# Optimization experiments

Measured on AMD Instinct MI355X. Metric: run time of the kernel, lower is better.

## Reference

```python
import jax, jax.numpy as jnp
import numpy as np
from math import sqrt

B, LQ, LK = 4, 256, 50000
EDGE_IN, NODE_IN, OUT = 128, 128, 256
KV_IN = NODE_IN + EDGE_IN  # 256


def setup_inputs() -> dict:
    key = jax.random.key(0)
    ks = jax.random.split(key, 8)
    s = 0.05
    return {
        "query": jax.random.normal(ks[0], (B, LQ, EDGE_IN), jnp.float32),
        "input": jax.random.normal(ks[1], (B, LK, KV_IN), jnp.float32),
        "Wq": jax.random.normal(ks[2], (OUT, EDGE_IN), jnp.float32) * s,
        "bq": jax.random.normal(ks[3], (OUT,), jnp.float32) * s,
        "Wk": jax.random.normal(ks[4], (OUT, KV_IN), jnp.float32) * s,
        "bk": jax.random.normal(ks[5], (OUT,), jnp.float32) * s,
        "Wv": jax.random.normal(ks[6], (OUT, KV_IN), jnp.float32) * s,
        "bv": jax.random.normal(ks[7], (OUT,), jnp.float32) * s,
    }


def reference(query, input, Wq, bq, Wk, bk, Wv, bv):
    norm = 1.0 / sqrt(OUT)
    Q = query @ Wq.T + bq            # [B, LQ, OUT]
    K = input @ Wk.T + bk            # [B, LK, OUT]
    V = input @ Wv.T + bv            # [B, LK, OUT]
    alpha = jnp.einsum("bqd,bkd->bqk", Q, K) * norm  # [B, LQ, LK]
    alpha = jax.nn.softmax(alpha, axis=-1)
    # z = alpha^T * V broadcasts only because LQ == OUT:
    # out[b, j] = sum_k alpha[b, j, k] * V[b, k, j]
    return jnp.einsum("bqk,bkq->bq", alpha, V)      # [B, OUT]
```

## Files before the change

### kernel.cpp

```cpp
#include <hip/hip_runtime.h>
#include <hip/hip_bf16.h>
#include <stdint.h>

using f32x4  = __attribute__((ext_vector_type(4))) float;
using bf16x8 = __attribute__((ext_vector_type(8))) short;

constexpr int BATCH = 4;
constexpr int LQ_   = 256;
constexpr int LK_   = 50000;
constexpr int OUTD  = 256;
constexpr int EIN   = 128;
constexpr int TR    = 16;
constexpr int NT    = LK_ / TR;
constexpr int KCH   = 64;

__device__ __forceinline__ uint32_t f2bf(float f) {
  uint32_t u = __builtin_bit_cast(uint32_t, f);
  u = (u + 0x7fffu + ((u >> 16) & 1u)) >> 16;
  return u;
}

__device__ __forceinline__ void block_sync_lds() {
  asm volatile("s_waitcnt lgkmcnt(0)" ::: "memory");
  __builtin_amdgcn_sched_barrier(0);
  __builtin_amdgcn_s_barrier();
  __builtin_amdgcn_sched_barrier(0);
}

__global__ __launch_bounds__(256) void prep_all(
    const float* __restrict__ query, const float* __restrict__ Wq,
    const float* __restrict__ bq,    const float* __restrict__ Wk,
    const float* __restrict__ Wv,    ushort* __restrict__ Gn,
    ushort* __restrict__ Wvbf,       float* __restrict__ numden)
{
  const int blk = blockIdx.x, tid = threadIdx.x;
  if (blk >= 64) {
    if (blk < 96) {
      int base = (blk - 64) * 2048 + tid * 8;
      float4 a = *(const float4*)(Wv + base);
      float4 c = *(const float4*)(Wv + base + 4);
      uint4 pk;
      pk.x = f2bf(a.x) | (f2bf(a.y) << 16);
      pk.y = f2bf(a.z) | (f2bf(a.w) << 16);
      pk.z = f2bf(c.x) | (f2bf(c.y) << 16);
      pk.w = f2bf(c.z) | (f2bf(c.w) << 16);
      *(uint4*)(Wvbf + base) = pk;
    } else {
      for (int i = tid; i < 2 * BATCH * OUTD; i += 256) numden[i] = 0.f;
    }
    return;
  }
  __shared__ float qin[16 * EIN];
  __shared__ float Qr [16 * OUTD];
  const int b = blk >> 4, q0 = (blk & 15) * 16;
  {
    int idx = tid * 8;
    int row = idx >> 7, c = idx & 127;
    const float* p = query + ((size_t)b * LQ_ + q0 + row) * EIN + c;
    float4 a = *(const float4*)p;
    float4 d = *(const float4*)(p + 4);
    float* q = &qin[row * EIN + c];
    q[0]=a.x; q[1]=a.y; q[2]=a.z; q[3]=a.w; q[4]=d.x; q[5]=d.y; q[6]=d.z; q[7]=d.w;
  }
  __syncthreads();

  float acc[16];
  {
    float bias = bq[tid];
#pragma unroll
    for (int i = 0; i < 16; ++i) acc[i] = bias;
  }
  for (int d4 = 0; d4 < EIN / 4; ++d4) {
    f32x4 w4 = *(const f32x4*)(Wq + tid * EIN + d4 * 4);
#pragma unroll
    for (int i = 0; i < 16; ++i) {
      f32x4 q4 = *(const f32x4*)(qin + i * EIN + d4 * 4);
      acc[i] += q4[0]*w4[0] + q4[1]*w4[1] + q4[2]*w4[2] + q4[3]*w4[3];
    }
  }
#pragma unroll
  for (int i = 0; i < 16; ++i) Qr[i * OUTD + tid] = acc[i];
  __syncthreads();

  float acc2[16];
#pragma unroll
  for (int i = 0; i < 16; ++i) acc2[i] = 0.f;
  for (int d4 = 0; d4 < OUTD / 4; ++d4) {
    float w0 = Wk[(d4*4+0) * OUTD + tid];
    float w1 = Wk[(d4*4+1) * OUTD + tid];
    float w2 = Wk[(d4*4+2) * OUTD + tid];
    float w3 = Wk[(d4*4+3) * OUTD + tid];
#pragma unroll
    for (int i = 0; i < 16; ++i) {
      f32x4 q4 = *(const f32x4*)(Qr + i * OUTD + d4 * 4);
      acc2[i] += q4[0]*w0 + q4[1]*w1 + q4[2]*w2 + q4[3]*w3;
    }
  }
  const float norm = 0.0625f;
#pragma unroll
  for (int i = 0; i < 16; ++i)
    Gn[((size_t)b * LQ_ + q0 + i) * OUTD + tid] = (ushort)f2bf(acc2[i] * norm);
}

__global__ __launch_bounds__(1024, 4) void attn_main(
    const float*  __restrict__ input, const ushort* __restrict__ Gn,
    const ushort* __restrict__ Wvbf,  float* __restrict__ num,
    float* __restrict__ den)
{
  __shared__ ushort in_lds[2 * 4096];
  const int idx = blockIdx.x;
  const int b = idx >> 6, kch = idx & (KCH - 1);
  const int t0 = (kch * NT) >> 6, t1 = ((kch + 1) * NT) >> 6;
  const int tid = threadIdx.x, w = tid >> 6, l = tid & 63;
  const int lg = l >> 4, lr = l & 15;
  const float* src = input + (size_t)b * LK_ * 256;

  const int arow = w * 16 + lr;
  const ushort* gp = Gn   + ((size_t)b * LQ_ + arow) * 256 + lg * 8;
  const ushort* vp = Wvbf + (size_t)arow * 256 + lg * 8;
  bf16x8 ga[8], wa[8];
#pragma unroll
  for (int k = 0; k < 8; ++k) {
    ga[k] = *(const bf16x8*)(gp + k * 32);
    wa[k] = *(const bf16x8*)(vp + k * 32);
    asm volatile("" : "+v"(ga[k]), "+v"(wa[k]));
  }

  float numr[4], denr[4];
#pragma unroll
  for (int r = 0; r < 4; ++r) { numr[r] = 0.f; denr[r] = 0.f; }

  const int sg = tid >> 1, sh = tid & 1;
  const int srow = sg >> 5, sfbg = sg & 31;
  float4 s0;
  auto loadreg = [&](int t) {
    const float* p = src + (size_t)(t * TR + srow) * 256 + sfbg * 8 + sh * 4;
    s0 = *(const float4*)p;
  };
  auto writebuf = [&](int buf) {
    char* base = (char*)in_lds + buf * 8192;
    uint2 pk;
    pk.x = f2bf(s0.x) | (f2bf(s0.y) << 16);
    pk.y = f2bf(s0.z) | (f2bf(s0.w) << 16);
    *(uint2*)(base + sfbg * 256 + ((srow ^ (sfbg & 15)) << 4) + sh * 8) = pk;
  };

  loadreg(t0);
  writebuf(t0 & 1);
  loadreg(t0 + 1);
  block_sync_lds();

  for (int t = t0; t < t1; ++t) {
    const char* bbuf = (const char*)in_lds + (t & 1) * 8192;
    f32x4 aS = {0,0,0,0};
    f32x4 aV = {0,0,0,0};
#pragma unroll
    for (int ks = 0; ks < 8; ++ks) {
      const int fb = ks * 4 + lg;
      bf16x8 bb = *(const bf16x8*)(bbuf + fb * 256 + ((lr ^ (fb & 15)) << 4));
      aS = __builtin_amdgcn_mfma_f32_16x16x32_bf16(ga[ks], bb, aS, 0, 0, 0);
      aV = __builtin_amdgcn_mfma_f32_16x16x32_bf16(wa[ks], bb, aV, 0, 0, 0);
    }
#pragma unroll
    for (int r = 0; r < 4; ++r) {
      float e = __expf(aS[r]);
      denr[r] += e;
      numr[r] += e * aV[r];
    }
    if (t + 1 < t1) {
      writebuf((t + 1) & 1);
      if (t + 2 < t1) loadreg(t + 2);
    }
    block_sync_lds();
  }

#pragma unroll
  for (int r = 0; r < 4; ++r) {
    float d_ = denr[r], n_ = numr[r];
#pragma unroll
    for (int m = 1; m < 16; m <<= 1) {
      d_ += __shfl_xor(d_, m, 64);
      n_ += __shfl_xor(n_, m, 64);
    }
    if (lr == 0) {
      int q = w * 16 + lg * 4 + r;
      atomicAdd(&den[b * OUTD + q], d_);
      atomicAdd(&num[b * OUTD + q], n_);
    }
  }
}

__global__ __launch_bounds__(256) void finalize(const float* __restrict__ num,
                                                const float* __restrict__ den,
                                                const float* __restrict__ bv,
                                                float* __restrict__ out) {
  int i = blockIdx.x * 256 + threadIdx.x;
  out[i] = num[i] / den[i] + bv[i & 255];
}

extern "C" void kernel_launch(void* const* d_in, const int* in_sizes, int n_in,
                              void* d_out, int out_size, void* d_ws, size_t ws_size,
                              hipStream_t stream)
{
  const float* query = (const float*)d_in[0];
  const float* input = (const float*)d_in[1];
  const float* Wq    = (const float*)d_in[2];
  const float* bq    = (const float*)d_in[3];
  const float* Wk    = (const float*)d_in[4];
  const float* Wv    = (const float*)d_in[6];
  const float* bv    = (const float*)d_in[7];
  float* out = (float*)d_out;

  char* ws = (char*)d_ws;
  ushort* Gn     = (ushort*)ws;
  ushort* Wvbf   = (ushort*)(ws + 524288);
  float*  numden = (float*)(ws + 524288 + 131072);
  float*  num    = numden;
  float*  den    = numden + BATCH * OUTD;

  prep_all<<<97, 256, 0, stream>>>(query, Wq, bq, Wk, Wv, Gn, Wvbf, numden);
  attn_main<<<BATCH * KCH, 1024, 0, stream>>>(input, Gn, Wvbf, num, den);
  finalize<<<BATCH, 256, 0, stream>>>(num, den, bv, out);
}
```

Before: 105.6 us.

## Split query rows across two 512-thread blocks and use hardware bf16 pack conversion

```diff
diff --git a/kernel.cpp b/kernel.cpp
--- a/kernel.cpp
+++ b/kernel.cpp
@@ -18,6 +18,11 @@
   uint32_t u = __builtin_bit_cast(uint32_t, f);
   u = (u + 0x7fffu + ((u >> 16) & 1u)) >> 16;
   return u;
+}
+__device__ __forceinline__ uint32_t cvtpk(float lo, float hi) {
+  uint32_t r;
+  asm volatile("v_cvt_pk_bf16_f32 %0, %1, %2" : "=v"(r) : "v"(lo), "v"(hi));
+  return r;
 }
 
 __device__ __forceinline__ void block_sync_lds() {
@@ -102,20 +107,20 @@
     Gn[((size_t)b * LQ_ + q0 + i) * OUTD + tid] = (ushort)f2bf(acc2[i] * norm);
 }
 
-__global__ __launch_bounds__(1024, 4) void attn_main(
+__global__ __launch_bounds__(512, 4) void attn_main(
     const float*  __restrict__ input, const ushort* __restrict__ Gn,
     const ushort* __restrict__ Wvbf,  float* __restrict__ num,
     float* __restrict__ den)
 {
   __shared__ ushort in_lds[2 * 4096];
   const int idx = blockIdx.x;
-  const int b = idx >> 6, kch = idx & (KCH - 1);
+  const int b = idx >> 7, qb = (idx >> 6) & 1, kch = idx & (KCH - 1);
   const int t0 = (kch * NT) >> 6, t1 = ((kch + 1) * NT) >> 6;
   const int tid = threadIdx.x, w = tid >> 6, l = tid & 63;
   const int lg = l >> 4, lr = l & 15;
   const float* src = input + (size_t)b * LK_ * 256;
 
-  const int arow = w * 16 + lr;
+  const int arow = qb * 128 + w * 16 + lr;
   const ushort* gp = Gn   + ((size_t)b * LQ_ + arow) * 256 + lg * 8;
   const ushort* vp = Wvbf + (size_t)arow * 256 + lg * 8;
   bf16x8 ga[8], wa[8];
@@ -130,19 +135,24 @@
 #pragma unroll
   for (int r = 0; r < 4; ++r) { numr[r] = 0.f; denr[r] = 0.f; }
 
-  const int sg = tid >> 1, sh = tid & 1;
-  const int srow = sg >> 5, sfbg = sg & 31;
-  float4 s0;
+  const int srow = tid >> 5, sfbg = tid & 31;
+  const float* sbase = src + sfbg * 8;
+  float4 s0, s1;
   auto loadreg = [&](int t) {
-    const float* p = src + (size_t)(t * TR + srow) * 256 + sfbg * 8 + sh * 4;
+    int row = t * TR + srow;
+    row = row < LK_ ? row : LK_ - 1;
+    const float* p = sbase + (size_t)row * 256;
     s0 = *(const float4*)p;
+    s1 = *(const float4*)(p + 4);
   };
   auto writebuf = [&](int buf) {
     char* base = (char*)in_lds + buf * 8192;
-    uint2 pk;
-    pk.x = f2bf(s0.x) | (f2bf(s0.y) << 16);
-    pk.y = f2bf(s0.z) | (f2bf(s0.w) << 16);
-    *(uint2*)(base + sfbg * 256 + ((srow ^ (sfbg & 15)) << 4) + sh * 8) = pk;
+    uint4 pk;
+    pk.x = cvtpk(s0.x, s0.y);
+    pk.y = cvtpk(s0.z, s0.w);
+    pk.z = cvtpk(s1.x, s1.y);
+    pk.w = cvtpk(s1.z, s1.w);
+    *(uint4*)(base + sfbg * 256 + ((srow ^ (sfbg & 15)) << 4)) = pk;
   };
 
   loadreg(t0);
@@ -183,7 +193,7 @@
       n_ += __shfl_xor(n_, m, 64);
     }
     if (lr == 0) {
-      int q = w * 16 + lg * 4 + r;
+      int q = qb * 128 + w * 16 + lg * 4 + r;
       atomicAdd(&den[b * OUTD + q], d_);
       atomicAdd(&num[b * OUTD + q], n_);
     }
@@ -219,6 +229,6 @@
   float*  den    = numden + BATCH * OUTD;
 
   prep_all<<<97, 256, 0, stream>>>(query, Wq, bq, Wk, Wv, Gn, Wvbf, numden);
-  attn_main<<<BATCH * KCH, 1024, 0, stream>>>(input, Gn, Wvbf, num, den);
+  attn_main<<<BATCH * 2 * KCH, 512, 0, stream>>>(input, Gn, Wvbf, num, den);
   finalize<<<BATCH, 256, 0, stream>>>(num, den, bv, out);
 }
```

Result: slower. 109.4 us (+3.6%).

## Fuse finalize into attention via last-block counter; split prep G computation wider

Applied to the files above, without the earlier changes.

```diff
diff --git a/kernel.cpp b/kernel.cpp
--- a/kernel.cpp
+++ b/kernel.cpp
@@ -27,16 +27,17 @@
   __builtin_amdgcn_sched_barrier(0);
 }
 
-__global__ __launch_bounds__(256) void prep_all(
+__global__ __launch_bounds__(256) void prep_fused(
     const float* __restrict__ query, const float* __restrict__ Wq,
     const float* __restrict__ bq,    const float* __restrict__ Wk,
     const float* __restrict__ Wv,    ushort* __restrict__ Gn,
-    ushort* __restrict__ Wvbf,       float* __restrict__ numden)
+    ushort* __restrict__ Wvbf,       float* __restrict__ numden,
+    int* __restrict__ cnt)
 {
   const int blk = blockIdx.x, tid = threadIdx.x;
-  if (blk >= 64) {
-    if (blk < 96) {
-      int base = (blk - 64) * 2048 + tid * 8;
+  if (blk >= 256) {
+    if (blk < 288) {
+      int base = (blk - 256) * 2048 + tid * 8;
       float4 a = *(const float4*)(Wv + base);
       float4 c = *(const float4*)(Wv + base + 4);
       uint4 pk;
@@ -47,12 +48,13 @@
       *(uint4*)(Wvbf + base) = pk;
     } else {
       for (int i = tid; i < 2 * BATCH * OUTD; i += 256) numden[i] = 0.f;
+      if (tid < BATCH) cnt[tid] = 0;
     }
     return;
   }
   __shared__ float qin[16 * EIN];
   __shared__ float Qr [16 * OUTD];
-  const int b = blk >> 4, q0 = (blk & 15) * 16;
+  const int b = blk >> 6, q0 = ((blk >> 2) & 15) * 16, colg = blk & 3;
   {
     int idx = tid * 8;
     int row = idx >> 7, c = idx & 127;
@@ -82,32 +84,27 @@
   for (int i = 0; i < 16; ++i) Qr[i * OUTD + tid] = acc[i];
   __syncthreads();
 
-  float acc2[16];
-#pragma unroll
-  for (int i = 0; i < 16; ++i) acc2[i] = 0.f;
-  for (int d4 = 0; d4 < OUTD / 4; ++d4) {
-    float w0 = Wk[(d4*4+0) * OUTD + tid];
-    float w1 = Wk[(d4*4+1) * OUTD + tid];
-    float w2 = Wk[(d4*4+2) * OUTD + tid];
-    float w3 = Wk[(d4*4+3) * OUTD + tid];
-#pragma unroll
-    for (int i = 0; i < 16; ++i) {
-      f32x4 q4 = *(const f32x4*)(Qr + i * OUTD + d4 * 4);
-      acc2[i] += q4[0]*w0 + q4[1]*w1 + q4[2]*w2 + q4[3]*w3;
-    }
-  }
-  const float norm = 0.0625f;
-#pragma unroll
-  for (int i = 0; i < 16; ++i)
-    Gn[((size_t)b * LQ_ + q0 + i) * OUTD + tid] = (ushort)f2bf(acc2[i] * norm);
+  const int col = colg * 64 + (tid & 63), rg = tid >> 6;
+  float acc2[4] = {0.f, 0.f, 0.f, 0.f};
+  for (int d = 0; d < OUTD; ++d) {
+    float wv = Wk[d * OUTD + col];
+#pragma unroll
+    for (int i = 0; i < 4; ++i) acc2[i] += Qr[(rg * 4 + i) * OUTD + d] * wv;
+  }
+  const float nrm = 1.4426950408889634f * 0.0625f;
+#pragma unroll
+  for (int i = 0; i < 4; ++i)
+    Gn[((size_t)b * LQ_ + q0 + rg * 4 + i) * OUTD + col] = (ushort)f2bf(acc2[i] * nrm);
 }
 
 __global__ __launch_bounds__(1024, 4) void attn_main(
     const float*  __restrict__ input, const ushort* __restrict__ Gn,
     const ushort* __restrict__ Wvbf,  float* __restrict__ num,
-    float* __restrict__ den)
+    float* __restrict__ den,          const float* __restrict__ bv,
+    int* __restrict__ cnt,            float* __restrict__ out)
 {
   __shared__ ushort in_lds[2 * 4096];
+  __shared__ int last_flag;
   const int idx = blockIdx.x;
   const int b = idx >> 6, kch = idx & (KCH - 1);
   const int t0 = (kch * NT) >> 6, t1 = ((kch + 1) * NT) >> 6;
@@ -163,7 +160,7 @@
     }
 #pragma unroll
     for (int r = 0; r < 4; ++r) {
-      float e = __expf(aS[r]);
+      float e = exp2f(aS[r]);
       denr[r] += e;
       numr[r] += e * aV[r];
     }
@@ -188,14 +185,16 @@
       atomicAdd(&num[b * OUTD + q], n_);
     }
   }
-}
-
-__global__ __launch_bounds__(256) void finalize(const float* __restrict__ num,
-                                                const float* __restrict__ den,
-                                                const float* __restrict__ bv,
-                                                float* __restrict__ out) {
-  int i = blockIdx.x * 256 + threadIdx.x;
-  out[i] = num[i] / den[i] + bv[i & 255];
+
+  __threadfence();
+  if (tid == 0)
+    last_flag = (atomicAdd(&cnt[b], 1) == KCH - 1) ? 1 : 0;
+  __syncthreads();
+  if (last_flag && tid < OUTD) {
+    float n_ = atomicAdd(&num[b * OUTD + tid], 0.f);
+    float d_ = atomicAdd(&den[b * OUTD + tid], 0.f);
+    out[b * OUTD + tid] = n_ / d_ + bv[tid];
+  }
 }
 
 extern "C" void kernel_launch(void* const* d_in, const int* in_sizes, int n_in,
@@ -217,8 +216,8 @@
   float*  numden = (float*)(ws + 524288 + 131072);
   float*  num    = numden;
   float*  den    = numden + BATCH * OUTD;
-
-  prep_all<<<97, 256, 0, stream>>>(query, Wq, bq, Wk, Wv, Gn, Wvbf, numden);
-  attn_main<<<BATCH * KCH, 1024, 0, stream>>>(input, Gn, Wvbf, num, den);
-  finalize<<<BATCH, 256, 0, stream>>>(num, den, bv, out);
-}
+  int*    cnt    = (int*)(ws + 524288 + 131072 + 8192);
+
+  prep_fused<<<289, 256, 0, stream>>>(query, Wq, bq, Wk, Wv, Gn, Wvbf, numden, cnt);
+  attn_main<<<BATCH * KCH, 1024, 0, stream>>>(input, Gn, Wvbf, num, den, bv, cnt, out);
+}
```

New measurement: 148.5 us. +40.7%, slower.
